# Performance work log

Measured on AMD Instinct MI355X. Metric: run time of the kernel, lower is better.

## Reference

```python
import jax, jax.numpy as jnp
import numpy as np

B, N_PER, D, L, DEG = 16, 2048, 128, 4, 16
N = B * N_PER
E = N * DEG
MSG_EPS = 1e-7  # GENConv message eps


def _lin_init(k, fi, fo):
    kw, kb = jax.random.split(k)
    s = 1.0 / np.sqrt(fi)
    W = jax.random.uniform(kw, (fi, fo), jnp.float32, minval=-s, maxval=s)
    b = jax.random.uniform(kb, (fo,), jnp.float32, minval=-s, maxval=s)
    return W, b


def setup_inputs() -> dict:
    key = jax.random.key(0)
    ks = jax.random.split(key, 6 + 2 * L)
    flat_c = jax.random.normal(ks[0], (N,), jnp.float32)
    edge_weight = jax.random.normal(ks[1], (E,), jnp.float32)
    # edges confined within each graph: local indices + per-graph offset
    e_per = N_PER * DEG
    local = jax.random.randint(ks[2], (2, B, e_per), 0, N_PER, jnp.int32)
    offs = (jnp.arange(B, dtype=jnp.int32) * N_PER)[None, :, None]
    edge_index = (local + offs).reshape(2, E)
    node_W, node_b = _lin_init(ks[3], 1, D)
    edge_W, edge_b = _lin_init(ks[4], 1, D)
    W1l, b1l, W2l, b2l = [], [], [], []
    for i in range(L):
        w1, bb1 = _lin_init(ks[6 + 2 * i], D, 2 * D)
        w2, bb2 = _lin_init(ks[7 + 2 * i], 2 * D, D)
        W1l.append(w1); b1l.append(bb1); W2l.append(w2); b2l.append(bb2)
    lin_W, lin_b = _lin_init(ks[5], D, 1)
    return dict(
        flat_c=flat_c, edge_weight=edge_weight, edge_index=edge_index,
        node_W=node_W, node_b=node_b, edge_W=edge_W, edge_b=edge_b,
        ts=jnp.ones((L,), jnp.float32),
        W1=jnp.stack(W1l), b1=jnp.stack(b1l),
        g1=jnp.ones((L, 2 * D), jnp.float32), be1=jnp.zeros((L, 2 * D), jnp.float32),
        W2=jnp.stack(W2l), b2=jnp.stack(b2l),
        ln_g=jnp.ones((L, D), jnp.float32), ln_b=jnp.zeros((L, D), jnp.float32),
        lin_W=lin_W, lin_b=lin_b)


def _layernorm(x, g, b, eps=1e-5):
    mu = jnp.mean(x, -1, keepdims=True)
    var = jnp.mean((x - mu) ** 2, -1, keepdims=True)
    return (x - mu) * jax.lax.rsqrt(var + eps) * g + b


def _gen_conv(x, edge_attr, src, dst, t, W1, b1, g1, be1, W2, b2):
    # GENConv with softmax aggregation (per-destination, per-channel)
    m = jax.nn.relu(x[src] + edge_attr) + MSG_EPS          # [E, D]
    logits = m * t
    mx = jax.ops.segment_max(logits, dst, num_segments=N)  # [N, D]
    ex = jnp.exp(logits - mx[dst])
    denom = jax.ops.segment_sum(ex, dst, num_segments=N)
    alpha = ex / (denom[dst] + 1e-16)
    aggr = jax.ops.segment_sum(m * alpha, dst, num_segments=N)  # [N, D]
    h = aggr + x
    # MLP: Linear(D,2D) -> LayerNorm -> ReLU -> Linear(2D,D)
    h = jax.nn.relu(_layernorm(h @ W1 + b1, g1, be1))
    return h @ W2 + b2


def reference(flat_c, edge_weight, edge_index, node_W, node_b, edge_W, edge_b,
              ts, W1, b1, g1, be1, W2, b2, ln_g, ln_b, lin_W, lin_b):
    src, dst = edge_index[0], edge_index[1]
    x = flat_c[:, None] @ node_W + node_b              # [N, D]
    ea = edge_weight[:, None] @ edge_W + edge_b        # [E, D]
    # first layer: raw conv only (pre-activation 'res+' scheme)
    x = _gen_conv(x, ea, src, dst, ts[0], W1[0], b1[0], g1[0], be1[0], W2[0], b2[0])
    for l in range(1, L):
        h = x
        z = jax.nn.relu(_layernorm(x, ln_g[l], ln_b[l]))  # dropout=identity (eval)
        x = _gen_conv(z, ea, src, dst, ts[l], W1[l], b1[l], g1[l], be1[l], W2[l], b2[l]) + h
    x = jax.nn.relu(_layernorm(x, ln_g[0], ln_b[0]))
    x = x @ lin_W + lin_b                              # [N, 1]
    out = x.reshape(B, N_PER)                          # equal-size graphs, max_len = N_PER
    return out - out[:, :1]                            # subtract first-node output per graph
```

## Files before the change

### kernel.cpp

```cpp
#include <hip/hip_runtime.h>
#include <hip/hip_bf16.h>
#include <stdint.h>

#define NN   32768
#define EE   524288
#define DD   128
#define D2   256
#define NPER 2048

using f32x4 = __attribute__((ext_vector_type(4))) float;
using sh8   = __attribute__((ext_vector_type(8))) short;
using sh4   = __attribute__((ext_vector_type(4))) short;

__device__ inline uint32_t rtn_hi_bits(float x){
  uint32_t u = __float_as_uint(x);
  return (u + 0x7FFFu + ((u >> 16) & 1u)) & 0xFFFF0000u;
}

__device__ inline int swz_node(int blk, int wave){
  int s = (blk & 7) * 1024 + (blk >> 3);
  return s * 4 + wave;
}

__global__ void k_count(const int* __restrict__ dst, int* __restrict__ cnt){
  int e = blockIdx.x * 256 + threadIdx.x;
  if (e < EE) atomicAdd(&cnt[dst[e]], 1);
}

__global__ __launch_bounds__(1024)
void k_scan(const int* __restrict__ cnt, int* __restrict__ rowptr){
  __shared__ int ps[1024];
  int t = threadIdx.x;
  int loc[32];
  int base = t * 32;
  int s = 0;
  #pragma unroll
  for (int j = 0; j < 32; ++j){ loc[j] = cnt[base + j]; s += loc[j]; }
  ps[t] = s; __syncthreads();
  for (int off = 1; off < 1024; off <<= 1){
    int v = (t >= off) ? ps[t - off] : 0;
    __syncthreads();
    ps[t] += v;
    __syncthreads();
  }
  int run = ps[t] - s;
  #pragma unroll
  for (int j = 0; j < 32; ++j){ rowptr[base + j] = run; run += loc[j]; }
  if (t == 1023) rowptr[NN] = run;
}

__global__ void k_scatter(const int* __restrict__ src, const int* __restrict__ dst,
                          const float* __restrict__ w, const int* __restrict__ rowptr,
                          int* __restrict__ cur, int* __restrict__ es, float* __restrict__ ew){
  int e = blockIdx.x * 256 + threadIdx.x;
  if (e < EE){
    int d = dst[e];
    int pos = rowptr[d] + atomicAdd(&cur[d], 1);
    es[pos] = src[e];
    ew[pos] = w[e];
  }
}

__global__ __launch_bounds__(256)
void k_packw(const float* __restrict__ W1, const float* __restrict__ W2,
             ushort* __restrict__ W1h, ushort* __restrict__ W1l,
             ushort* __restrict__ W2h, ushort* __restrict__ W2l){
  if (blockIdx.x < 64){
    int t = blockIdx.x * 256 + threadIdx.x;
    int lane = t & 63, mt = (t >> 6) & 15, kt = (t >> 10) & 3, layer = t >> 12;
    int nl = lane & 15, g = lane >> 4;
    int ucol = mt * 16 + nl;
    const float* Wp = W1 + layer * (DD * D2);
    sh8 hh, ll;
    #pragma unroll
    for (int j = 0; j < 8; ++j){
      int k = kt * 32 + g * 4 + (j & 3) + 16 * (j >> 2);
      float v = Wp[k * D2 + ucol];
      uint32_t hb = rtn_hi_bits(v);
      hh[j] = (short)(hb >> 16);
      ll[j] = (short)(__float_as_uint(v - __uint_as_float(hb)) >> 16);
    }
    *(sh8*)(W1h + t * 8) = hh;
    *(sh8*)(W1l + t * 8) = ll;
  } else {
    int t = (blockIdx.x - 64) * 256 + threadIdx.x;
    int lane = t & 63, mt = (t >> 6) & 7, kt = (t >> 9) & 7, layer = t >> 12;
    int nl = lane & 15, g = lane >> 4;
    int xcol = mt * 16 + nl;
    const float* Wp = W2 + layer * (D2 * DD);
    sh8 hh, ll;
    #pragma unroll
    for (int j = 0; j < 8; ++j){
      int k = kt * 32 + g * 4 + (j & 3) + 16 * (j >> 2);
      float v = Wp[k * DD + xcol];
      uint32_t hb = rtn_hi_bits(v);
      hh[j] = (short)(hb >> 16);
      ll[j] = (short)(__float_as_uint(v - __uint_as_float(hb)) >> 16);
    }
    *(sh8*)(W2h + t * 8) = hh;
    *(sh8*)(W2l + t * 8) = ll;
  }
}

template<int MODE>
__global__ __launch_bounds__(256)
void k_edge(const float* __restrict__ Zf, const float* __restrict__ cvec,
            const float* __restrict__ nW, const float* __restrict__ nb,
            const int* __restrict__ rowptr,
            const int* __restrict__ es, const float* __restrict__ ew,
            const float* __restrict__ eW, const float* __restrict__ eB,
            const float* __restrict__ ts, int layer,
            ushort* __restrict__ Hh, ushort* __restrict__ Hl){
  int n  = swz_node(blockIdx.x, threadIdx.x >> 6);
  int ld = threadIdx.x & 63;
  int d0 = ld * 2;
  float t  = ts[layer];
  float wx = eW[d0], wy = eW[d0 + 1];
  float bx = eB[d0], by = eB[d0 + 1];
  float nwx = 0.f, nwy = 0.f, nbx = 0.f, nby = 0.f;
  if (MODE == 0){ nwx = nW[d0]; nwy = nW[d0 + 1]; nbx = nb[d0]; nby = nb[d0 + 1]; }
  int r0 = __builtin_amdgcn_readfirstlane(rowptr[n]);
  int r1 = __builtin_amdgcn_readfirstlane(rowptr[n + 1]);

  float s0a = 0.f, s1a = 0.f, a0a = 0.f, a1a = 0.f;

  auto body = [&](float zx, float zy, float wj){
    float m0 = fmaxf(zx + fmaf(wj, wx, bx), 0.f) + 1e-7f;
    float m1 = fmaxf(zy + fmaf(wj, wy, by), 0.f) + 1e-7f;
    float p0 = __expf(fminf(m0 * t, 60.f));
    float p1 = __expf(fminf(m1 * t, 60.f));
    s0a += p0; a0a = fmaf(p0, m0, a0a);
    s1a += p1; a1a = fmaf(p1, m1, a1a);
  };

  int j = r0;
  for (; j + 4 <= r1; j += 4){
    int   sA = es[j],     sB = es[j + 1], sC = es[j + 2], sD = es[j + 3];
    float wA = ew[j],     wB = ew[j + 1], wC = ew[j + 2], wD = ew[j + 3];
    float zAx, zAy, zBx, zBy, zCx, zCy, zDx, zDy;
    if (MODE == 0){
      float cA = cvec[sA], cB = cvec[sB], cC = cvec[sC], cD = cvec[sD];
      zAx = fmaf(cA, nwx, nbx); zAy = fmaf(cA, nwy, nby);
      zBx = fmaf(cB, nwx, nbx); zBy = fmaf(cB, nwy, nby);
      zCx = fmaf(cC, nwx, nbx); zCy = fmaf(cC, nwy, nby);
      zDx = fmaf(cD, nwx, nbx); zDy = fmaf(cD, nwy, nby);
    } else {
      float2 zA = *(const float2*)(Zf + (size_t)sA * DD + d0);
      float2 zB = *(const float2*)(Zf + (size_t)sB * DD + d0);
      float2 zC = *(const float2*)(Zf + (size_t)sC * DD + d0);
      float2 zD = *(const float2*)(Zf + (size_t)sD * DD + d0);
      zAx = zA.x; zAy = zA.y; zBx = zB.x; zBy = zB.y;
      zCx = zC.x; zCy = zC.y; zDx = zD.x; zDy = zD.y;
    }
    body(zAx, zAy, wA); body(zBx, zBy, wB);
    body(zCx, zCy, wC); body(zDx, zDy, wD);
  }
  for (; j < r1; ++j){
    int s = es[j]; float w = ew[j];
    float zx, zy;
    if (MODE == 0){
      float cs = cvec[s];
      zx = fmaf(cs, nwx, nbx); zy = fmaf(cs, nwy, nby);
    } else {
      float2 z = *(const float2*)(Zf + (size_t)s * DD + d0);
      zx = z.x; zy = z.y;
    }
    body(zx, zy, w);
  }

  float znx, zny;
  if (MODE == 0){
    float cn = cvec[n];
    znx = fmaf(cn, nwx, nbx); zny = fmaf(cn, nwy, nby);
  } else {
    float2 zn2 = *(const float2*)(Zf + (size_t)n * DD + d0);
    znx = zn2.x; zny = zn2.y;
  }
  float hx = fmaf(a0a, __builtin_amdgcn_rcpf(s0a + 1e-16f), znx);
  float hy = fmaf(a1a, __builtin_amdgcn_rcpf(s1a + 1e-16f), zny);
  uint32_t hbx = rtn_hi_bits(hx), hby = rtn_hi_bits(hy);
  uint32_t hw = (hbx >> 16) | (hby & 0xFFFF0000u);
  float lx = hx - __uint_as_float(hbx), ly = hy - __uint_as_float(hby);
  uint32_t lw = (__float_as_uint(lx) >> 16) | (__float_as_uint(ly) & 0xFFFF0000u);
  ((uint32_t*)(Hh + (size_t)n * DD))[ld] = hw;
  ((uint32_t*)(Hl + (size_t)n * DD))[ld] = lw;
}

__global__ __launch_bounds__(256, 2)
void k_mlp(const ushort* __restrict__ Hhi, const ushort* __restrict__ Hlo,
           const ushort* __restrict__ W1h, const ushort* __restrict__ W1l,
           const float* __restrict__ b1, const float* __restrict__ g1,
           const float* __restrict__ be1,
           const ushort* __restrict__ W2h, const ushort* __restrict__ W2l,
           const float* __restrict__ b2, const float* __restrict__ Xres,
           float* __restrict__ Xout,
           const float* __restrict__ lnG, const float* __restrict__ lnB,
           float* __restrict__ Zout, int hasRes, int writeX)
{
  __shared__ ushort Ufh[16384];
  __shared__ ushort Ufl[16384];
  __shared__ float2 Pln[256];

  const int tid = threadIdx.x;
  const int w = tid >> 6, l = tid & 63, nl = l & 15, g = l >> 4;
  const int bs = (blockIdx.x & 7) * 64 + (blockIdx.x >> 3);
  const int n0 = bs * 64;

  f32x4 acc[4][4];
  #pragma unroll
  for (int mi = 0; mi < 4; ++mi)
    #pragma unroll
    for (int nt = 0; nt < 4; ++nt) acc[mi][nt] = (f32x4)0.f;

  const int hbase = (n0 + nl) * DD + g * 4;

  #pragma unroll
  for (int kt = 0; kt < 4; ++kt){
    sh8 ah[4], al[4];
    #pragma unroll
    for (int mi = 0; mi < 4; ++mi){
      int fi = ((kt * 16 + w * 4 + mi) * 64 + l) * 8;
      ah[mi] = *(const sh8*)(W1h + fi);
      al[mi] = *(const sh8*)(W1l + fi);
    }
    sh8 bh[4], bl[4];
    #pragma unroll
    for (int nt = 0; nt < 4; ++nt){
      int hi_ = hbase + nt * 16 * DD + kt * 32;
      sh8 vh, vl;
      ((sh4*)&vh)[0] = *(const sh4*)(Hhi + hi_);
      ((sh4*)&vh)[1] = *(const sh4*)(Hhi + hi_ + 16);
      ((sh4*)&vl)[0] = *(const sh4*)(Hlo + hi_);
      ((sh4*)&vl)[1] = *(const sh4*)(Hlo + hi_ + 16);
      bh[nt] = vh; bl[nt] = vl;
    }
    #pragma unroll
    for (int mi = 0; mi < 4; ++mi)
      #pragma unroll
      for (int nt = 0; nt < 4; ++nt){
        acc[mi][nt] = __builtin_amdgcn_mfma_f32_16x16x32_bf16(ah[mi], bh[nt], acc[mi][nt], 0, 0, 0);
        acc[mi][nt] = __builtin_amdgcn_mfma_f32_16x16x32_bf16(ah[mi], bl[nt], acc[mi][nt], 0, 0, 0);
        acc[mi][nt] = __builtin_amdgcn_mfma_f32_16x16x32_bf16(al[mi], bh[nt], acc[mi][nt], 0, 0, 0);
      }
  }

  #pragma unroll
  for (int mi = 0; mi < 4; ++mi){
    f32x4 bv = *(const f32x4*)(b1 + w * 64 + mi * 16 + g * 4);
    #pragma unroll
    for (int nt = 0; nt < 4; ++nt) acc[mi][nt] += bv;
  }
  float s1[4], s2[4];
  #pragma unroll
  for (int nt = 0; nt < 4; ++nt){
    float a = 0.f, b = 0.f;
    #pragma unroll
    for (int mi = 0; mi < 4; ++mi)
      #pragma unroll
      for (int r = 0; r < 4; ++r){ float v = acc[mi][nt][r]; a += v; b += v * v; }
    a += __shfl_xor(a, 16); b += __shfl_xor(b, 16);
    a += __shfl_xor(a, 32); b += __shfl_xor(b, 32);
    s1[nt] = a; s2[nt] = b;
  }
  {
    float p1 = (g == 0) ? s1[0] : (g == 1) ? s1[1] : (g == 2) ? s1[2] : s1[3];
    float p2 = (g == 0) ? s2[0] : (g == 1) ? s2[1] : (g == 2) ? s2[2] : s2[3];
    Pln[(g * 16 + nl) * 4 + w] = make_float2(p1, p2);
  }
  __syncthreads();

  {
    f32x4 gv[4], ev[4];
    #pragma unroll
    for (int mi = 0; mi < 4; ++mi){
      gv[mi] = *(const f32x4*)(g1  + w * 64 + mi * 16 + g * 4);
      ev[mi] = *(const f32x4*)(be1 + w * 64 + mi * 16 + g * 4);
    }
    #pragma unroll
    for (int nt = 0; nt < 4; ++nt){
      int node = nt * 16 + nl;
      float t1 = 0.f, t2 = 0.f;
      #pragma unroll
      for (int wi = 0; wi < 4; ++wi){
        float2 pp = Pln[node * 4 + wi];
        t1 += pp.x; t2 += pp.y;
      }
      float mean = t1 * (1.f / D2);
      float var  = t2 * (1.f / D2) - mean * mean;
      float rstd = 1.f / sqrtf(var + 1e-5f);
      #pragma unroll
      for (int p = 0; p < 2; ++p){
        sh8 uh, ul;
        #pragma unroll
        for (int j = 0; j < 8; ++j){
          int mi = 2 * p + (j >> 2), r = j & 3;
          float v = (acc[mi][nt][r] - mean) * rstd * gv[mi][r] + ev[mi][r];
          v = fmaxf(v, 0.f);
          uint32_t hb = rtn_hi_bits(v);
          uh[j] = (short)(hb >> 16);
          ul[j] = (short)(__float_as_uint(v - __uint_as_float(hb)) >> 16);
        }
        int fo = (((2 * w + p) * 4 + nt) * 64 + l) * 8;
        *(sh8*)(Ufh + fo) = uh;
        *(sh8*)(Ufl + fo) = ul;
      }
    }
  }
  __syncthreads();

  f32x4 a2[2][4];
  #pragma unroll
  for (int mi = 0; mi < 2; ++mi)
    #pragma unroll
    for (int nt = 0; nt < 4; ++nt) a2[mi][nt] = (f32x4)0.f;
  #pragma unroll
  for (int kt = 0; kt < 8; ++kt){
    sh8 wh[2], wl[2];
    #pragma unroll
    for (int mi = 0; mi < 2; ++mi){
      int fi = ((kt * 8 + w * 2 + mi) * 64 + l) * 8;
      wh[mi] = *(const sh8*)(W2h + fi);
      wl[mi] = *(const sh8*)(W2l + fi);
    }
    sh8 uh[4], ul[4];
    #pragma unroll
    for (int nt = 0; nt < 4; ++nt){
      int fo = ((kt * 4 + nt) * 64 + l) * 8;
      uh[nt] = *(const sh8*)(Ufh + fo);
      ul[nt] = *(const sh8*)(Ufl + fo);
    }
    #pragma unroll
    for (int mi = 0; mi < 2; ++mi)
      #pragma unroll
      for (int nt = 0; nt < 4; ++nt){
        a2[mi][nt] = __builtin_amdgcn_mfma_f32_16x16x32_bf16(wh[mi], uh[nt], a2[mi][nt], 0, 0, 0);
        a2[mi][nt] = __builtin_amdgcn_mfma_f32_16x16x32_bf16(wh[mi], ul[nt], a2[mi][nt], 0, 0, 0);
        a2[mi][nt] = __builtin_amdgcn_mfma_f32_16x16x32_bf16(wl[mi], uh[nt], a2[mi][nt], 0, 0, 0);
      }
  }
  __syncthreads();

  float* Xb = (float*)Ufh;
  #pragma unroll
  for (int mi = 0; mi < 2; ++mi)
    #pragma unroll
    for (int nt = 0; nt < 4; ++nt){
      int node = nt * 16 + nl;
      int xc = (w * 2 + mi) * 16 + g * 4;
      int idx = node * DD + (xc ^ ((node & 7) << 2));
      *(f32x4*)(Xb + idx) = a2[mi][nt];
    }
  __syncthreads();

  {
    int en = tid >> 2, ec = tid & 3;
    f32x4 vr[8];
    float s1e = 0.f, s2e = 0.f;
    #pragma unroll
    for (int i = 0; i < 8; ++i){
      int q = ec + i * 4;
      int c = q * 4;
      int idx = en * DD + ((q ^ (en & 7)) << 2);
      f32x4 v = *(const f32x4*)(Xb + idx);
      v += *(const f32x4*)(b2 + c);
      if (hasRes) v += *(const f32x4*)(Xres + (size_t)(n0 + en) * DD + c);
      vr[i] = v;
      #pragma unroll
      for (int r = 0; r < 4; ++r){ s1e += v[r]; s2e += v[r] * v[r]; }
    }
    s1e += __shfl_xor(s1e, 1); s2e += __shfl_xor(s2e, 1);
    s1e += __shfl_xor(s1e, 2); s2e += __shfl_xor(s2e, 2);
    float mean = s1e * (1.f / DD);
    float var  = s2e * (1.f / DD) - mean * mean;
    float rs   = 1.f / sqrtf(var + 1e-5f);
    #pragma unroll
    for (int i = 0; i < 8; ++i){
      int q = ec + i * 4;
      int c = q * 4;
      if (writeX) *(f32x4*)(Xout + (size_t)(n0 + en) * DD + c) = vr[i];
      f32x4 gv = *(const f32x4*)(lnG + c);
      f32x4 bv = *(const f32x4*)(lnB + c);
      f32x4 z;
      #pragma unroll
      for (int r = 0; r < 4; ++r)
        z[r] = fmaxf((vr[i][r] - mean) * rs * gv[r] + bv[r], 0.f);
      *(f32x4*)(Zout + (size_t)(n0 + en) * DD + c) = z;
    }
  }
}

__global__ __launch_bounds__(256)
void k_fin(const float* __restrict__ Zf, const float* __restrict__ linW,
           float* __restrict__ out){
  int n  = swz_node(blockIdx.x, threadIdx.x >> 6);
  int d0 = (threadIdx.x & 63) * 2;
  int nb_ = n & ~(NPER - 1);
  float2 v  = *(const float2*)(Zf + (size_t)n  * DD + d0);
  float2 vb = *(const float2*)(Zf + (size_t)nb_ * DD + d0);
  float2 lw = *(const float2*)(linW + d0);
  float p = (v.x - vb.x) * lw.x + (v.y - vb.y) * lw.y;
  #pragma unroll
  for (int m = 1; m < 64; m <<= 1) p += __shfl_xor(p, m);
  if ((threadIdx.x & 63) == 0) out[n] = p;
}

extern "C" void kernel_launch(void* const* d_in, const int* in_sizes, int n_in,
                              void* d_out, int out_size, void* d_ws, size_t ws_size,
                              hipStream_t stream){
  const float* flat_c = (const float*)d_in[0];
  const float* edge_w = (const float*)d_in[1];
  const int*   eidx   = (const int*)  d_in[2];
  const float* nodeW  = (const float*)d_in[3];
  const float* nodeB  = (const float*)d_in[4];
  const float* edgeW  = (const float*)d_in[5];
  const float* edgeB  = (const float*)d_in[6];
  const float* ts     = (const float*)d_in[7];
  const float* W1     = (const float*)d_in[8];
  const float* b1     = (const float*)d_in[9];
  const float* g1     = (const float*)d_in[10];
  const float* be1    = (const float*)d_in[11];
  const float* W2     = (const float*)d_in[12];
  const float* b2     = (const float*)d_in[13];
  const float* lng    = (const float*)d_in[14];
  const float* lnb    = (const float*)d_in[15];
  const float* linW   = (const float*)d_in[16];
  float* out = (float*)d_out;

  char* wsp = (char*)d_ws;
  size_t off = 0;
  auto alloc = [&](size_t bytes) -> void* {
    void* p = wsp + off;
    off += (bytes + 255) & ~(size_t)255;
    return p;
  };
  float*  bufA = (float*) alloc((size_t)NN * DD * 4);
  float*  bufB = (float*) alloc((size_t)NN * DD * 4);
  ushort* Hhi  = (ushort*)alloc((size_t)NN * DD * 2);
  ushort* Hlo  = (ushort*)alloc((size_t)NN * DD * 2);
  ushort* W1h  = (ushort*)alloc((size_t)4 * 32768 * 2);
  ushort* W1l  = (ushort*)alloc((size_t)4 * 32768 * 2);
  ushort* W2h  = (ushort*)alloc((size_t)4 * 32768 * 2);
  ushort* W2l  = (ushort*)alloc((size_t)4 * 32768 * 2);
  int*   cnt   = (int*)  alloc((size_t)NN * 4);
  int*   cur   = (int*)  alloc((size_t)NN * 4);
  int*   rowpt = (int*)  alloc((size_t)(NN + 1) * 4);
  int*   es    = (int*)  alloc((size_t)EE * 4);
  float* ewS   = (float*)alloc((size_t)EE * 4);
  if (off > ws_size) return;

  const int* srcI = eidx;
  const int* dstI = eidx + EE;

  (void)hipMemsetAsync(cnt, 0, (size_t)2 * NN * 4, stream);
  k_count  <<<EE / 256, 256, 0, stream>>>(dstI, cnt);
  k_scan   <<<1, 1024, 0, stream>>>(cnt, rowpt);
  k_scatter<<<EE / 256, 256, 0, stream>>>(srcI, dstI, edge_w, rowpt, cur, es, ewS);
  k_packw  <<<128, 256, 0, stream>>>(W1, W2, W1h, W1l, W2h, W2l);

  for (int l = 0; l < 4; ++l){
    if (l == 0)
      k_edge<0><<<NN / 4, 256, 0, stream>>>(nullptr, flat_c, nodeW, nodeB,
                                            rowpt, es, ewS, edgeW, edgeB, ts, l, Hhi, Hlo);
    else
      k_edge<1><<<NN / 4, 256, 0, stream>>>(bufA, nullptr, nullptr, nullptr,
                                            rowpt, es, ewS, edgeW, edgeB, ts, l, Hhi, Hlo);
    int nx = (l + 1) & 3;
    k_mlp <<<NN / 64, 256, 0, stream>>>(Hhi, Hlo,
                                        W1h + (size_t)l * 32768, W1l + (size_t)l * 32768,
                                        b1 + l * D2, g1 + l * D2, be1 + l * D2,
                                        W2h + (size_t)l * 32768, W2l + (size_t)l * 32768,
                                        b2 + l * DD, bufB, bufB,
                                        lng + nx * DD, lnb + nx * DD, bufA,
                                        l > 0 ? 1 : 0, l < 3 ? 1 : 0);
  }
  k_fin<<<NN / 4, 256, 0, stream>>>(bufA, linW, out);
}
```

Before: 308.6 us.

## Fuse edge aggregation into MLP kernel and fold final projection into last layer

```diff
diff --git a/kernel.cpp b/kernel.cpp
--- a/kernel.cpp
+++ b/kernel.cpp
@@ -15,11 +15,6 @@
 __device__ inline uint32_t rtn_hi_bits(float x){
   uint32_t u = __float_as_uint(x);
   return (u + 0x7FFFu + ((u >> 16) & 1u)) & 0xFFFF0000u;
-}
-
-__device__ inline int swz_node(int blk, int wave){
-  int s = (blk & 7) * 1024 + (blk >> 3);
-  return s * 4 + wave;
 }
 
 __global__ void k_count(const int* __restrict__ dst, int* __restrict__ cnt){
@@ -103,99 +98,24 @@
 }
 
 template<int MODE>
-__global__ __launch_bounds__(256)
-void k_edge(const float* __restrict__ Zf, const float* __restrict__ cvec,
-            const float* __restrict__ nW, const float* __restrict__ nb,
-            const int* __restrict__ rowptr,
-            const int* __restrict__ es, const float* __restrict__ ew,
-            const float* __restrict__ eW, const float* __restrict__ eB,
-            const float* __restrict__ ts, int layer,
-            ushort* __restrict__ Hh, ushort* __restrict__ Hl){
-  int n  = swz_node(blockIdx.x, threadIdx.x >> 6);
-  int ld = threadIdx.x & 63;
-  int d0 = ld * 2;
-  float t  = ts[layer];
-  float wx = eW[d0], wy = eW[d0 + 1];
-  float bx = eB[d0], by = eB[d0 + 1];
-  float nwx = 0.f, nwy = 0.f, nbx = 0.f, nby = 0.f;
-  if (MODE == 0){ nwx = nW[d0]; nwy = nW[d0 + 1]; nbx = nb[d0]; nby = nb[d0 + 1]; }
-  int r0 = __builtin_amdgcn_readfirstlane(rowptr[n]);
-  int r1 = __builtin_amdgcn_readfirstlane(rowptr[n + 1]);
-
-  float s0a = 0.f, s1a = 0.f, a0a = 0.f, a1a = 0.f;
-
-  auto body = [&](float zx, float zy, float wj){
-    float m0 = fmaxf(zx + fmaf(wj, wx, bx), 0.f) + 1e-7f;
-    float m1 = fmaxf(zy + fmaf(wj, wy, by), 0.f) + 1e-7f;
-    float p0 = __expf(fminf(m0 * t, 60.f));
-    float p1 = __expf(fminf(m1 * t, 60.f));
-    s0a += p0; a0a = fmaf(p0, m0, a0a);
-    s1a += p1; a1a = fmaf(p1, m1, a1a);
-  };
-
-  int j = r0;
-  for (; j + 4 <= r1; j += 4){
-    int   sA = es[j],     sB = es[j + 1], sC = es[j + 2], sD = es[j + 3];
-    float wA = ew[j],     wB = ew[j + 1], wC = ew[j + 2], wD = ew[j + 3];
-    float zAx, zAy, zBx, zBy, zCx, zCy, zDx, zDy;
-    if (MODE == 0){
-      float cA = cvec[sA], cB = cvec[sB], cC = cvec[sC], cD = cvec[sD];
-      zAx = fmaf(cA, nwx, nbx); zAy = fmaf(cA, nwy, nby);
-      zBx = fmaf(cB, nwx, nbx); zBy = fmaf(cB, nwy, nby);
-      zCx = fmaf(cC, nwx, nbx); zCy = fmaf(cC, nwy, nby);
-      zDx = fmaf(cD, nwx, nbx); zDy = fmaf(cD, nwy, nby);
-    } else {
-      float2 zA = *(const float2*)(Zf + (size_t)sA * DD + d0);
-      float2 zB = *(const float2*)(Zf + (size_t)sB * DD + d0);
-      float2 zC = *(const float2*)(Zf + (size_t)sC * DD + d0);
-      float2 zD = *(const float2*)(Zf + (size_t)sD * DD + d0);
-      zAx = zA.x; zAy = zA.y; zBx = zB.x; zBy = zB.y;
-      zCx = zC.x; zCy = zC.y; zDx = zD.x; zDy = zD.y;
-    }
-    body(zAx, zAy, wA); body(zBx, zBy, wB);
-    body(zCx, zCy, wC); body(zDx, zDy, wD);
-  }
-  for (; j < r1; ++j){
-    int s = es[j]; float w = ew[j];
-    float zx, zy;
-    if (MODE == 0){
-      float cs = cvec[s];
-      zx = fmaf(cs, nwx, nbx); zy = fmaf(cs, nwy, nby);
-    } else {
-      float2 z = *(const float2*)(Zf + (size_t)s * DD + d0);
-      zx = z.x; zy = z.y;
-    }
-    body(zx, zy, w);
-  }
-
-  float znx, zny;
-  if (MODE == 0){
-    float cn = cvec[n];
-    znx = fmaf(cn, nwx, nbx); zny = fmaf(cn, nwy, nby);
-  } else {
-    float2 zn2 = *(const float2*)(Zf + (size_t)n * DD + d0);
-    znx = zn2.x; zny = zn2.y;
-  }
-  float hx = fmaf(a0a, __builtin_amdgcn_rcpf(s0a + 1e-16f), znx);
-  float hy = fmaf(a1a, __builtin_amdgcn_rcpf(s1a + 1e-16f), zny);
-  uint32_t hbx = rtn_hi_bits(hx), hby = rtn_hi_bits(hy);
-  uint32_t hw = (hbx >> 16) | (hby & 0xFFFF0000u);
-  float lx = hx - __uint_as_float(hbx), ly = hy - __uint_as_float(hby);
-  uint32_t lw = (__float_as_uint(lx) >> 16) | (__float_as_uint(ly) & 0xFFFF0000u);
-  ((uint32_t*)(Hh + (size_t)n * DD))[ld] = hw;
-  ((uint32_t*)(Hl + (size_t)n * DD))[ld] = lw;
-}
-
 __global__ __launch_bounds__(256, 2)
-void k_mlp(const ushort* __restrict__ Hhi, const ushort* __restrict__ Hlo,
-           const ushort* __restrict__ W1h, const ushort* __restrict__ W1l,
-           const float* __restrict__ b1, const float* __restrict__ g1,
-           const float* __restrict__ be1,
-           const ushort* __restrict__ W2h, const ushort* __restrict__ W2l,
-           const float* __restrict__ b2, const float* __restrict__ Xres,
-           float* __restrict__ Xout,
-           const float* __restrict__ lnG, const float* __restrict__ lnB,
-           float* __restrict__ Zout, int hasRes, int writeX)
+void k_layer(const float* __restrict__ Zf, const float* __restrict__ cvec,
+             const float* __restrict__ nW, const float* __restrict__ nb,
+             const int* __restrict__ rowptr,
+             const int* __restrict__ es, const float* __restrict__ ew,
+             const float* __restrict__ eW, const float* __restrict__ eB,
+             const float* __restrict__ ts, int layer,
+             ushort* __restrict__ Hh, ushort* __restrict__ Hl,
+             const ushort* __restrict__ W1h, const ushort* __restrict__ W1l,
+             const float* __restrict__ b1, const float* __restrict__ g1,
+             const float* __restrict__ be1,
+             const ushort* __restrict__ W2h, const ushort* __restrict__ W2l,
+             const float* __restrict__ b2, const float* __restrict__ Xres,
+             float* __restrict__ Xout,
+             const float* __restrict__ lnG, const float* __restrict__ lnB,
+             float* __restrict__ Zout,
+             const float* __restrict__ linW, float* __restrict__ yv,
+             int hasRes, int writeX, int doFin)
 {
   __shared__ ushort Ufh[16384];
   __shared__ ushort Ufl[16384];
@@ -206,6 +126,79 @@
   const int bs = (blockIdx.x & 7) * 64 + (blockIdx.x >> 3);
   const int n0 = bs * 64;
 
+  {
+    int d0 = l * 2;
+    float t  = ts[layer];
+    float wx = eW[d0], wy = eW[d0 + 1];
+    float bx = eB[d0], by = eB[d0 + 1];
+    float nwx = 0.f, nwy = 0.f, nbx = 0.f, nby = 0.f;
+    if (MODE == 0){ nwx = nW[d0]; nwy = nW[d0 + 1]; nbx = nb[d0]; nby = nb[d0 + 1]; }
+    for (int i = 0; i < 16; ++i){
+      int n = n0 + w * 16 + i;
+      int r0 = __builtin_amdgcn_readfirstlane(rowptr[n]);
+      int r1 = __builtin_amdgcn_readfirstlane(rowptr[n + 1]);
+      float s0a = 0.f, s1a = 0.f, a0a = 0.f, a1a = 0.f;
+
+      auto body = [&](float zx, float zy, float wj){
+        float m0 = fmaxf(zx + fmaf(wj, wx, bx), 0.f) + 1e-7f;
+        float m1 = fmaxf(zy + fmaf(wj, wy, by), 0.f) + 1e-7f;
+        float p0 = __expf(fminf(m0 * t, 60.f));
+        float p1 = __expf(fminf(m1 * t, 60.f));
+        s0a += p0; a0a = fmaf(p0, m0, a0a);
+        s1a += p1; a1a = fmaf(p1, m1, a1a);
+      };
+
+      int j = r0;
+      for (; j + 8 <= r1; j += 8){
+        float zx[8], zy[8], wv[8];
+        #pragma unroll
+        for (int u = 0; u < 8; ++u){
+          int s = es[j + u]; wv[u] = ew[j + u];
+          if (MODE == 0){
+            float cs = cvec[s];
+            zx[u] = fmaf(cs, nwx, nbx); zy[u] = fmaf(cs, nwy, nby);
+          } else {
+            float2 z = *(const float2*)(Zf + (size_t)s * DD + d0);
+            zx[u] = z.x; zy[u] = z.y;
+          }
+        }
+        #pragma unroll
+        for (int u = 0; u < 8; ++u) body(zx[u], zy[u], wv[u]);
+      }
+      for (; j < r1; ++j){
+        int s = es[j]; float wj = ew[j];
+        float zx, zy;
+        if (MODE == 0){
+          float cs = cvec[s];
+          zx = fmaf(cs, nwx, nbx); zy = fmaf(cs, nwy, nby);
+        } else {
+          float2 z = *(const float2*)(Zf + (size_t)s * DD + d0);
+          zx = z.x; zy = z.y;
+        }
+        body(zx, zy, wj);
+      }
+
+      float znx, zny;
+      if (MODE == 0){
+        float cn = cvec[n];
+        znx = fmaf(cn, nwx, nbx); zny = fmaf(cn, nwy, nby);
+      } else {
+        float2 zn2 = *(const float2*)(Zf + (size_t)n * DD + d0);
+        znx = zn2.x; zny = zn2.y;
+      }
+      float hx = fmaf(a0a, __builtin_amdgcn_rcpf(s0a + 1e-16f), znx);
+      float hy = fmaf(a1a, __builtin_amdgcn_rcpf(s1a + 1e-16f), zny);
+      uint32_t hbx = rtn_hi_bits(hx), hby = rtn_hi_bits(hy);
+      uint32_t hw = (hbx >> 16) | (hby & 0xFFFF0000u);
+      float lx = hx - __uint_as_float(hbx), ly = hy - __uint_as_float(hby);
+      uint32_t lw = (__float_as_uint(lx) >> 16) | (__float_as_uint(ly) & 0xFFFF0000u);
+      ((uint32_t*)(Hh + (size_t)n * DD))[l] = hw;
+      ((uint32_t*)(Hl + (size_t)n * DD))[l] = lw;
+    }
+  }
+  __threadfence_block();
+  __syncthreads();
+
   f32x4 acc[4][4];
   #pragma unroll
   for (int mi = 0; mi < 4; ++mi)
@@ -228,10 +221,10 @@
     for (int nt = 0; nt < 4; ++nt){
       int hi_ = hbase + nt * 16 * DD + kt * 32;
       sh8 vh, vl;
-      ((sh4*)&vh)[0] = *(const sh4*)(Hhi + hi_);
-      ((sh4*)&vh)[1] = *(const sh4*)(Hhi + hi_ + 16);
-      ((sh4*)&vl)[0] = *(const sh4*)(Hlo + hi_);
-      ((sh4*)&vl)[1] = *(const sh4*)(Hlo + hi_ + 16);
+      ((sh4*)&vh)[0] = *(const sh4*)(Hh + hi_);
+      ((sh4*)&vh)[1] = *(const sh4*)(Hh + hi_ + 16);
+      ((sh4*)&vl)[0] = *(const sh4*)(Hl + hi_);
+      ((sh4*)&vl)[1] = *(const sh4*)(Hl + hi_ + 16);
       bh[nt] = vh; bl[nt] = vl;
     }
     #pragma unroll
@@ -373,6 +366,7 @@
     float mean = s1e * (1.f / DD);
     float var  = s2e * (1.f / DD) - mean * mean;
     float rs   = 1.f / sqrtf(var + 1e-5f);
+    float p = 0.f;
     #pragma unroll
     for (int i = 0; i < 8; ++i){
       int q = ec + i * 4;
@@ -384,24 +378,24 @@
       #pragma unroll
       for (int r = 0; r < 4; ++r)
         z[r] = fmaxf((vr[i][r] - mean) * rs * gv[r] + bv[r], 0.f);
-      *(f32x4*)(Zout + (size_t)(n0 + en) * DD + c) = z;
-    }
-  }
-}
-
-__global__ __launch_bounds__(256)
-void k_fin(const float* __restrict__ Zf, const float* __restrict__ linW,
-           float* __restrict__ out){
-  int n  = swz_node(blockIdx.x, threadIdx.x >> 6);
-  int d0 = (threadIdx.x & 63) * 2;
-  int nb_ = n & ~(NPER - 1);
-  float2 v  = *(const float2*)(Zf + (size_t)n  * DD + d0);
-  float2 vb = *(const float2*)(Zf + (size_t)nb_ * DD + d0);
-  float2 lw = *(const float2*)(linW + d0);
-  float p = (v.x - vb.x) * lw.x + (v.y - vb.y) * lw.y;
-  #pragma unroll
-  for (int m = 1; m < 64; m <<= 1) p += __shfl_xor(p, m);
-  if ((threadIdx.x & 63) == 0) out[n] = p;
+      if (doFin){
+        f32x4 lw = *(const f32x4*)(linW + c);
+        #pragma unroll
+        for (int r = 0; r < 4; ++r) p = fmaf(z[r], lw[r], p);
+      } else {
+        *(f32x4*)(Zout + (size_t)(n0 + en) * DD + c) = z;
+      }
+    }
+    if (doFin){
+      p += __shfl_xor(p, 1); p += __shfl_xor(p, 2);
+      if (ec == 0) yv[n0 + en] = p;
+    }
+  }
+}
+
+__global__ void k_fin2(const float* __restrict__ y, float* __restrict__ out){
+  int i = blockIdx.x * 256 + threadIdx.x;
+  out[i] = y[i] - y[i & ~(NPER - 1)];
 }
 
 extern "C" void kernel_launch(void* const* d_in, const int* in_sizes, int n_in,
@@ -446,6 +440,7 @@
   int*   rowpt = (int*)  alloc((size_t)(NN + 1) * 4);
   int*   es    = (int*)  alloc((size_t)EE * 4);
   float* ewS   = (float*)alloc((size_t)EE * 4);
+  float* y     = (float*)alloc((size_t)NN * 4);
   if (off > ws_size) return;
 
   const int* srcI = eidx;
@@ -458,20 +453,23 @@
   k_packw  <<<128, 256, 0, stream>>>(W1, W2, W1h, W1l, W2h, W2l);
 
   for (int l = 0; l < 4; ++l){
+    int nx = (l + 1) & 3;
     if (l == 0)
-      k_edge<0><<<NN / 4, 256, 0, stream>>>(nullptr, flat_c, nodeW, nodeB,
-                                            rowpt, es, ewS, edgeW, edgeB, ts, l, Hhi, Hlo);
+      k_layer<0><<<NN / 64, 256, 0, stream>>>(
+          nullptr, flat_c, nodeW, nodeB, rowpt, es, ewS, edgeW, edgeB, ts, l,
+          Hhi, Hlo,
+          W1h, W1l, b1, g1, be1, W2h, W2l, b2,
+          bufB, bufB, lng + nx * DD, lnb + nx * DD, bufA, linW, y,
+          0, 1, 0);
     else
-      k_edge<1><<<NN / 4, 256, 0, stream>>>(bufA, nullptr, nullptr, nullptr,
-                                            rowpt, es, ewS, edgeW, edgeB, ts, l, Hhi, Hlo);
-    int nx = (l + 1) & 3;
-    k_mlp <<<NN / 64, 256, 0, stream>>>(Hhi, Hlo,
-                                        W1h + (size_t)l * 32768, W1l + (size_t)l * 32768,
-                                        b1 + l * D2, g1 + l * D2, be1 + l * D2,
-                                        W2h + (size_t)l * 32768, W2l + (size_t)l * 32768,
-                                        b2 + l * DD, bufB, bufB,
-                                        lng + nx * DD, lnb + nx * DD, bufA,
-                                        l > 0 ? 1 : 0, l < 3 ? 1 : 0);
-  }
-  k_fin<<<NN / 4, 256, 0, stream>>>(bufA, linW, out);
-}
+      k_layer<1><<<NN / 64, 256, 0, stream>>>(
+          bufA, nullptr, nullptr, nullptr, rowpt, es, ewS, edgeW, edgeB, ts, l,
+          Hhi, Hlo,
+          W1h + (size_t)l * 32768, W1l + (size_t)l * 32768,
+          b1 + l * D2, g1 + l * D2, be1 + l * D2,
+          W2h + (size_t)l * 32768, W2l + (size_t)l * 32768, b2 + l * DD,
+          bufB, bufB, lng + nx * DD, lnb + nx * DD, bufA, linW, y,
+          1, l < 3 ? 1 : 0, l == 3 ? 1 : 0);
+  }
+  k_fin2<<<NN / 256, 256, 0, stream>>>(y, out);
+}
```

After: 359.7 us. +16.6%, slower.

## Split edge aggregation to one channel per lane and fuse count with weight packing

Applied to the files above, without the earlier changes.

```diff
diff --git a/kernel.cpp b/kernel.cpp
--- a/kernel.cpp
+++ b/kernel.cpp
@@ -15,16 +15,6 @@
 __device__ inline uint32_t rtn_hi_bits(float x){
   uint32_t u = __float_as_uint(x);
   return (u + 0x7FFFu + ((u >> 16) & 1u)) & 0xFFFF0000u;
-}
-
-__device__ inline int swz_node(int blk, int wave){
-  int s = (blk & 7) * 1024 + (blk >> 3);
-  return s * 4 + wave;
-}
-
-__global__ void k_count(const int* __restrict__ dst, int* __restrict__ cnt){
-  int e = blockIdx.x * 256 + threadIdx.x;
-  if (e < EE) atomicAdd(&cnt[dst[e]], 1);
 }
 
 __global__ __launch_bounds__(1024)
@@ -62,11 +52,16 @@
 }
 
 __global__ __launch_bounds__(256)
-void k_packw(const float* __restrict__ W1, const float* __restrict__ W2,
-             ushort* __restrict__ W1h, ushort* __restrict__ W1l,
-             ushort* __restrict__ W2h, ushort* __restrict__ W2l){
-  if (blockIdx.x < 64){
-    int t = blockIdx.x * 256 + threadIdx.x;
+void k_count_pack(const int* __restrict__ dst, int* __restrict__ cnt,
+                  const float* __restrict__ W1, const float* __restrict__ W2,
+                  ushort* __restrict__ W1h, ushort* __restrict__ W1l,
+                  ushort* __restrict__ W2h, ushort* __restrict__ W2l){
+  int b = blockIdx.x;
+  if (b < 2048){
+    int e = b * 256 + threadIdx.x;
+    atomicAdd(&cnt[dst[e]], 1);
+  } else if (b < 2112){
+    int t = (b - 2048) * 256 + threadIdx.x;
     int lane = t & 63, mt = (t >> 6) & 15, kt = (t >> 10) & 3, layer = t >> 12;
     int nl = lane & 15, g = lane >> 4;
     int ucol = mt * 16 + nl;
@@ -83,7 +78,7 @@
     *(sh8*)(W1h + t * 8) = hh;
     *(sh8*)(W1l + t * 8) = ll;
   } else {
-    int t = (blockIdx.x - 64) * 256 + threadIdx.x;
+    int t = (b - 2112) * 256 + threadIdx.x;
     int lane = t & 63, mt = (t >> 6) & 7, kt = (t >> 9) & 7, layer = t >> 12;
     int nl = lane & 15, g = lane >> 4;
     int xcol = mt * 16 + nl;
@@ -111,79 +106,59 @@
             const float* __restrict__ eW, const float* __restrict__ eB,
             const float* __restrict__ ts, int layer,
             ushort* __restrict__ Hh, ushort* __restrict__ Hl){
-  int n  = swz_node(blockIdx.x, threadIdx.x >> 6);
-  int ld = threadIdx.x & 63;
-  int d0 = ld * 2;
+  int wv = threadIdx.x >> 6;
+  int s2 = (blockIdx.x & 7) * 2048 + (blockIdx.x >> 3);
+  int n  = s2 * 2 + (wv >> 1);
+  int d0 = (wv & 1) * 64 + (threadIdx.x & 63);
   float t  = ts[layer];
-  float wx = eW[d0], wy = eW[d0 + 1];
-  float bx = eB[d0], by = eB[d0 + 1];
-  float nwx = 0.f, nwy = 0.f, nbx = 0.f, nby = 0.f;
-  if (MODE == 0){ nwx = nW[d0]; nwy = nW[d0 + 1]; nbx = nb[d0]; nby = nb[d0 + 1]; }
+  float wx = eW[d0], bx = eB[d0];
+  float nwx = 0.f, nbx = 0.f;
+  if (MODE == 0){ nwx = nW[d0]; nbx = nb[d0]; }
   int r0 = __builtin_amdgcn_readfirstlane(rowptr[n]);
   int r1 = __builtin_amdgcn_readfirstlane(rowptr[n + 1]);
 
-  float s0a = 0.f, s1a = 0.f, a0a = 0.f, a1a = 0.f;
-
-  auto body = [&](float zx, float zy, float wj){
+  float s0a = 0.f, a0a = 0.f;
+
+  auto body = [&](float zx, float wj){
     float m0 = fmaxf(zx + fmaf(wj, wx, bx), 0.f) + 1e-7f;
-    float m1 = fmaxf(zy + fmaf(wj, wy, by), 0.f) + 1e-7f;
     float p0 = __expf(fminf(m0 * t, 60.f));
-    float p1 = __expf(fminf(m1 * t, 60.f));
     s0a += p0; a0a = fmaf(p0, m0, a0a);
-    s1a += p1; a1a = fmaf(p1, m1, a1a);
   };
 
   int j = r0;
   for (; j + 4 <= r1; j += 4){
     int   sA = es[j],     sB = es[j + 1], sC = es[j + 2], sD = es[j + 3];
     float wA = ew[j],     wB = ew[j + 1], wC = ew[j + 2], wD = ew[j + 3];
-    float zAx, zAy, zBx, zBy, zCx, zCy, zDx, zDy;
+    float zA, zB, zC, zD;
     if (MODE == 0){
-      float cA = cvec[sA], cB = cvec[sB], cC = cvec[sC], cD = cvec[sD];
-      zAx = fmaf(cA, nwx, nbx); zAy = fmaf(cA, nwy, nby);
-      zBx = fmaf(cB, nwx, nbx); zBy = fmaf(cB, nwy, nby);
-      zCx = fmaf(cC, nwx, nbx); zCy = fmaf(cC, nwy, nby);
-      zDx = fmaf(cD, nwx, nbx); zDy = fmaf(cD, nwy, nby);
+      zA = fmaf(cvec[sA], nwx, nbx);
+      zB = fmaf(cvec[sB], nwx, nbx);
+      zC = fmaf(cvec[sC], nwx, nbx);
+      zD = fmaf(cvec[sD], nwx, nbx);
     } else {
-      float2 zA = *(const float2*)(Zf + (size_t)sA * DD + d0);
-      float2 zB = *(const float2*)(Zf + (size_t)sB * DD + d0);
-      float2 zC = *(const float2*)(Zf + (size_t)sC * DD + d0);
-      float2 zD = *(const float2*)(Zf + (size_t)sD * DD + d0);
-      zAx = zA.x; zAy = zA.y; zBx = zB.x; zBy = zB.y;
-      zCx = zC.x; zCy = zC.y; zDx = zD.x; zDy = zD.y;
-    }
-    body(zAx, zAy, wA); body(zBx, zBy, wB);
-    body(zCx, zCy, wC); body(zDx, zDy, wD);
+      zA = Zf[(size_t)sA * DD + d0];
+      zB = Zf[(size_t)sB * DD + d0];
+      zC = Zf[(size_t)sC * DD + d0];
+      zD = Zf[(size_t)sD * DD + d0];
+    }
+    body(zA, wA); body(zB, wB); body(zC, wC); body(zD, wD);
   }
   for (; j < r1; ++j){
     int s = es[j]; float w = ew[j];
-    float zx, zy;
-    if (MODE == 0){
-      float cs = cvec[s];
-      zx = fmaf(cs, nwx, nbx); zy = fmaf(cs, nwy, nby);
-    } else {
-      float2 z = *(const float2*)(Zf + (size_t)s * DD + d0);
-      zx = z.x; zy = z.y;
-    }
-    body(zx, zy, w);
-  }
-
-  float znx, zny;
-  if (MODE == 0){
-    float cn = cvec[n];
-    znx = fmaf(cn, nwx, nbx); zny = fmaf(cn, nwy, nby);
-  } else {
-    float2 zn2 = *(const float2*)(Zf + (size_t)n * DD + d0);
-    znx = zn2.x; zny = zn2.y;
-  }
+    float zx;
+    if (MODE == 0) zx = fmaf(cvec[s], nwx, nbx);
+    else           zx = Zf[(size_t)s * DD + d0];
+    body(zx, w);
+  }
+
+  float znx;
+  if (MODE == 0) znx = fmaf(cvec[n], nwx, nbx);
+  else           znx = Zf[(size_t)n * DD + d0];
   float hx = fmaf(a0a, __builtin_amdgcn_rcpf(s0a + 1e-16f), znx);
-  float hy = fmaf(a1a, __builtin_amdgcn_rcpf(s1a + 1e-16f), zny);
-  uint32_t hbx = rtn_hi_bits(hx), hby = rtn_hi_bits(hy);
-  uint32_t hw = (hbx >> 16) | (hby & 0xFFFF0000u);
-  float lx = hx - __uint_as_float(hbx), ly = hy - __uint_as_float(hby);
-  uint32_t lw = (__float_as_uint(lx) >> 16) | (__float_as_uint(ly) & 0xFFFF0000u);
-  ((uint32_t*)(Hh + (size_t)n * DD))[ld] = hw;
-  ((uint32_t*)(Hl + (size_t)n * DD))[ld] = lw;
+  uint32_t hbx = rtn_hi_bits(hx);
+  float lx = hx - __uint_as_float(hbx);
+  Hh[(size_t)n * DD + d0] = (ushort)(hbx >> 16);
+  Hl[(size_t)n * DD + d0] = (ushort)(__float_as_uint(lx) >> 16);
 }
 
 __global__ __launch_bounds__(256, 2)
@@ -392,7 +367,8 @@
 __global__ __launch_bounds__(256)
 void k_fin(const float* __restrict__ Zf, const float* __restrict__ linW,
            float* __restrict__ out){
-  int n  = swz_node(blockIdx.x, threadIdx.x >> 6);
+  int blk = blockIdx.x;
+  int n = ((blk & 7) * 1024 + (blk >> 3)) * 4 + (threadIdx.x >> 6);
   int d0 = (threadIdx.x & 63) * 2;
   int nb_ = n & ~(NPER - 1);
   float2 v  = *(const float2*)(Zf + (size_t)n  * DD + d0);
@@ -452,17 +428,16 @@
   const int* dstI = eidx + EE;
 
   (void)hipMemsetAsync(cnt, 0, (size_t)2 * NN * 4, stream);
-  k_count  <<<EE / 256, 256, 0, stream>>>(dstI, cnt);
+  k_count_pack<<<2176, 256, 0, stream>>>(dstI, cnt, W1, W2, W1h, W1l, W2h, W2l);
   k_scan   <<<1, 1024, 0, stream>>>(cnt, rowpt);
   k_scatter<<<EE / 256, 256, 0, stream>>>(srcI, dstI, edge_w, rowpt, cur, es, ewS);
-  k_packw  <<<128, 256, 0, stream>>>(W1, W2, W1h, W1l, W2h, W2l);
 
   for (int l = 0; l < 4; ++l){
     if (l == 0)
-      k_edge<0><<<NN / 4, 256, 0, stream>>>(nullptr, flat_c, nodeW, nodeB,
+      k_edge<0><<<NN / 2, 256, 0, stream>>>(nullptr, flat_c, nodeW, nodeB,
                                             rowpt, es, ewS, edgeW, edgeB, ts, l, Hhi, Hlo);
     else
-      k_edge<1><<<NN / 4, 256, 0, stream>>>(bufA, nullptr, nullptr, nullptr,
+      k_edge<1><<<NN / 2, 256, 0, stream>>>(bufA, nullptr, nullptr, nullptr,
                                             rowpt, es, ewS, edgeW, edgeB, ts, l, Hhi, Hlo);
     int nx = (l + 1) & 3;
     k_mlp <<<NN / 64, 256, 0, stream>>>(Hhi, Hlo,
```

Result: slower. 321.0 us (+4.0%).
